# Kernel optimization log

Measured on AMD Instinct MI355X. Metric: run time of the kernel, lower is better.

The kernel has to match this reference:

```python
import jax, jax.numpy as jnp
import numpy as np

N_HEAD = 16

def _alibi_slopes(num_heads):
    # m_i = (256 ** (1/num_heads)) ** -(i+1)
    x = (2.0 ** 8) ** (1.0 / num_heads)
    return jnp.asarray([1.0 / x ** (i + 1) for i in range(num_heads)], dtype=jnp.float32)

def setup_inputs() -> dict:
    key = jax.random.key(0)
    k1, k2 = jax.random.split(key)
    B, S, D = 2, 2048, 1024
    x = jax.random.normal(k1, (B, S, D), dtype=jnp.float32)
    W_kqv = jax.random.normal(k2, (D, 3 * D), dtype=jnp.float32) * 0.02
    return {"x": x, "W_kqv": W_kqv}

def reference(x, W_kqv):
    B, S, D = x.shape
    H = N_HEAD
    hd = D // H
    scale = jnp.sqrt(jnp.asarray(D, dtype=x.dtype))  # NOTE: sqrt(n_embd), per source
    kqv = x @ W_kqv                                   # [B,S,3D]
    k, q, v = jnp.split(kqv, 3, axis=-1)              # chunk order: key, query, value
    q = q.reshape(B, S, H, hd).transpose(0, 2, 1, 3)  # [B,H,S,hd]
    k = k.reshape(B, S, H, hd).transpose(0, 2, 1, 3)
    v = v.reshape(B, S, H, hd).transpose(0, 2, 1, 3)
    # ALiBi bias: m[h] * (j - i)
    pos = jnp.arange(S)
    rel = (pos[None, :] - pos[:, None]).astype(x.dtype)      # [S,S]
    m = _alibi_slopes(H).astype(x.dtype)                     # [H]
    bias = m[:, None, None] * rel                            # [H,S,S]
    score = jnp.einsum('bhqd,bhkd->bhqk', q, k) / scale + bias[None]
    causal = pos[None, :] <= pos[:, None]                    # [S,S] lower-tri
    score = jnp.where(causal[None, None], score, -jnp.inf)
    attn = jax.nn.softmax(score, axis=-1)                    # [B,H,S,S]
    out = jnp.einsum('bhqk,bhkd->bhqd', attn, v)
    out = out.transpose(0, 2, 1, 3).reshape(B, S, D)
    return (out, attn)
```

## Files before the change

### kernel.cpp

```cpp
#include <hip/hip_runtime.h>
#include <hip/hip_bf16.h>

typedef __attribute__((ext_vector_type(8))) short short8;
typedef __attribute__((ext_vector_type(4))) float f32x4;

static __device__ __forceinline__ unsigned short f2bf(float f) {
    unsigned int x = __float_as_uint(f);
    x += 0x7fffu + ((x >> 16) & 1u);
    return (unsigned short)(x >> 16);
}

static __device__ __forceinline__ void gld_lds16(const unsigned short* g, unsigned short* l) {
    __builtin_amdgcn_global_load_lds((const __attribute__((address_space(1))) void*)g,
                                     (__attribute__((address_space(3))) void*)l, 16, 0, 0);
}

__global__ __launch_bounds__(256) void cvt_x_kernel(const float* __restrict__ in,
                                                    unsigned short* __restrict__ outb,
                                                    int n4) {
    int i = blockIdx.x * 256 + threadIdx.x;
    if (i < n4) {
        f32x4 v = *(const f32x4*)(in + (size_t)i * 4);
        ushort4 o;
        o.x = f2bf(v[0]); o.y = f2bf(v[1]); o.z = f2bf(v[2]); o.w = f2bf(v[3]);
        *(ushort4*)(outb + (size_t)i * 4) = o;
    }
}

__global__ __launch_bounds__(256) void cvt_wt_kernel(const float* __restrict__ W,
                                                     unsigned short* __restrict__ WT) {
    __shared__ float t[64][65];
    const int n0 = blockIdx.x * 64;
    const int k0 = blockIdx.y * 64;
    const int tid = threadIdx.x;
#pragma unroll
    for (int i = 0; i < 16; ++i) {
        int lin = tid + i * 256;
        int rr = lin >> 6, cc = lin & 63;
        t[rr][cc] = W[(size_t)(k0 + rr) * 3072 + n0 + cc];
    }
    __syncthreads();
#pragma unroll
    for (int i = 0; i < 16; ++i) {
        int lin = tid + i * 256;
        int nn = lin >> 6, kk = lin & 63;
        WT[(size_t)(n0 + nn) * 1024 + k0 + kk] = f2bf(t[kk][nn]);
    }
}

__global__ __launch_bounds__(256) void gemm_kqv_kernel(
    const unsigned short* __restrict__ A,
    const unsigned short* __restrict__ BT,
    unsigned short* __restrict__ qb,
    unsigned short* __restrict__ kb,
    unsigned short* __restrict__ vtb) {
    __shared__ __attribute__((aligned(16))) unsigned short smem[2 * 128 * 72];
    unsigned short (*As)[64] = (unsigned short(*)[64])smem;
    unsigned short (*Bs)[64] = (unsigned short(*)[64])(smem + 128 * 64);
    const int tid = threadIdx.x;
    const int w = tid >> 6, lane = tid & 63;
    const int quad = lane >> 4, cl = lane & 15;

    const int wg = (int)blockIdx.x + 24 * (int)blockIdx.y;
    const int wgs = (wg & 7) * 96 + (wg >> 3);
    const int m0 = (wgs / 24) * 128, n0 = (wgs % 24) * 128;
    const int wm = (w >> 1) * 64, wn = (w & 1) * 64;

    const int srow = lane >> 3;
    const int schk = (lane & 7) ^ srow;
    const unsigned short* Ap = A + (size_t)(m0 + w * 32 + srow) * 1024 + schk * 8;
    const unsigned short* Bp = BT + (size_t)(n0 + w * 32 + srow) * 1024 + schk * 8;

    f32x4 acc[4][4] = {};

    for (int kk = 0; kk < 1024; kk += 64) {
#pragma unroll
        for (int i = 0; i < 4; ++i) {
            gld_lds16(Ap + kk + (size_t)i * 8 * 1024, &As[w * 32 + i * 8][0]);
            gld_lds16(Bp + kk + (size_t)i * 8 * 1024, &Bs[w * 32 + i * 8][0]);
        }
        __syncthreads();
#pragma unroll
        for (int kc = 0; kc < 2; ++kc) {
            short8 af[4], bfr[4];
#pragma unroll
            for (int i = 0; i < 4; ++i) {
                const int col = ((kc * 4 + quad) ^ (cl & 7)) * 8;
                af[i] = *(const short8*)&As[wm + i * 16 + cl][col];
                bfr[i] = *(const short8*)&Bs[wn + i * 16 + cl][col];
            }
#pragma unroll
            for (int im = 0; im < 4; ++im)
#pragma unroll
                for (int in = 0; in < 4; ++in)
                    acc[im][in] = __builtin_amdgcn_mfma_f32_16x16x32_bf16(
                        af[im], bfr[in], acc[im][in], 0, 0, 0);
        }
        __syncthreads();
    }
    unsigned short (*Cs)[130] = (unsigned short(*)[130])smem;

    const int chunk = n0 >> 10;
    const int d0 = n0 & 1023;
    const int b = m0 >> 11;
    const int s_base = m0 & 2047;

    if (chunk == 2) {
#pragma unroll
        for (int im = 0; im < 4; ++im)
#pragma unroll
            for (int in = 0; in < 4; ++in)
#pragma unroll
                for (int rg = 0; rg < 4; ++rg)
                    Cs[wn + in * 16 + cl][wm + im * 16 + quad * 4 + rg] =
                        f2bf(acc[im][in][rg]);
        __syncthreads();
#pragma unroll
        for (int it = 0; it < 8; ++it) {
            int l = it * 2048 + tid * 8;
            int c = l >> 7;
            int r = l & 127;
            int d = d0 + c, hh = d >> 6, dd = d & 63;
            size_t dst = ((size_t)(b * 16 + hh) * 64 + dd) * 2048 + s_base + r;
            *(uint4*)(vtb + dst) = *(const uint4*)&Cs[c][r];
        }
    } else {
#pragma unroll
        for (int im = 0; im < 4; ++im)
#pragma unroll
            for (int in = 0; in < 4; ++in)
#pragma unroll
                for (int rg = 0; rg < 4; ++rg)
                    Cs[wm + im * 16 + quad * 4 + rg][wn + in * 16 + cl] =
                        f2bf(acc[im][in][rg]);
        __syncthreads();
        unsigned short* outp = (chunk == 0) ? kb : qb;
#pragma unroll
        for (int it = 0; it < 8; ++it) {
            int l = it * 2048 + tid * 8;
            int r = l >> 7;
            int c = l & 127;
            int d = d0 + c, hh = d >> 6, dd = d & 63;
            size_t dst = ((size_t)(b * 16 + hh) * 2048 + s_base + r) * 64 + dd;
            *(uint4*)(outp + dst) = *(const uint4*)&Cs[r][c];
        }
    }
}

__global__ __launch_bounds__(128, 3) void attn_kernel(
    const unsigned short* __restrict__ qb,
    const unsigned short* __restrict__ kb,
    const unsigned short* __restrict__ vtb,
    float* __restrict__ out_,
    float* __restrict__ attn) {
    const int h = blockIdx.y;
    const int b = blockIdx.z;
    const int bh = b * 16 + h;
    const int t32 = (37 * (int)blockIdx.x + 11 * bh) & 63;
    const int tid = threadIdx.x;
    const int w = tid >> 6;
    const int lane = tid & 63;
    const int quad = lane >> 4;
    const int cl = lane & 15;
    const int q0 = t32 * 32;
    const int row0 = q0 + w * 16;
    const int jtmax = t32 >> 1;

    const unsigned short* Qh = qb + (size_t)bh * 2048 * 64;
    const unsigned short* Kh = kb + (size_t)bh * 2048 * 64;
    const unsigned short* Vh = vtb + (size_t)bh * 64 * 2048;
    float* attnh = attn + (size_t)bh * 2048 * 2048;

    short8 aq0 = *(const short8*)(Qh + (size_t)(row0 + cl) * 64 + quad * 8);
    short8 aq1 = *(const short8*)(Qh + (size_t)(row0 + cl) * 64 + 32 + quad * 8);

    const float LOG2E = 1.44269504088896f;
    const float C1 = LOG2E / 32.0f;
    const float M2 = exp2f(-0.5f * (float)(h + 1)) * LOG2E;

    auto loadK = [&](int jt, short8 (&kf)[8]) {
#pragma unroll
        for (int nt = 0; nt < 4; ++nt) {
            const unsigned short* Kp = Kh + (size_t)(jt * 64 + nt * 16 + cl) * 64 + quad * 8;
            kf[nt * 2] = *(const short8*)(Kp);
            kf[nt * 2 + 1] = *(const short8*)(Kp + 32);
        }
    };

    float rsum[4] = {0.f, 0.f, 0.f, 0.f};
    auto tile1 = [&](int jt, const short8 (&kf)[8]) {
        const int j0 = jt * 64;
#pragma unroll
        for (int nt = 0; nt < 4; ++nt) {
            f32x4 s = {0.f, 0.f, 0.f, 0.f};
            s = __builtin_amdgcn_mfma_f32_16x16x32_bf16(aq0, kf[nt * 2], s, 0, 0, 0);
            s = __builtin_amdgcn_mfma_f32_16x16x32_bf16(aq1, kf[nt * 2 + 1], s, 0, 0, 0);
            const int jc = j0 + nt * 16 + cl;
#pragma unroll
            for (int rg = 0; rg < 4; ++rg) {
                int irow = row0 + quad * 4 + rg;
                if (jc <= irow)
                    rsum[rg] += exp2f(s[rg] * C1 + M2 * (float)(jc - irow));
            }
        }
    };

    {
        short8 kf0[8], kf1[8];
        loadK(0, kf0);
        int jt = 0;
        for (;;) {
            if (jt < jtmax) loadK(jt + 1, kf1);
            tile1(jt, kf0);
            if (++jt > jtmax) break;
            if (jt < jtmax) loadK(jt + 1, kf0);
            tile1(jt, kf1);
            if (++jt > jtmax) break;
        }
    }
#pragma unroll
    for (int rg = 0; rg < 4; ++rg) {
        float v = rsum[rg];
        v += __shfl_xor(v, 1);
        v += __shfl_xor(v, 2);
        v += __shfl_xor(v, 4);
        v += __shfl_xor(v, 8);
        rsum[rg] = 1.0f / v;
    }

    __shared__ unsigned short Ps[2][16][72];
    f32x4 oacc[4] = {};
    short8 kf[8], vf[8];
    loadK(0, kf);
    for (int jt = 0; jt <= jtmax; ++jt) {
        const int j0 = jt * 64;
#pragma unroll
        for (int on = 0; on < 4; ++on) {
            const unsigned short* Vp = Vh + (size_t)(on * 16 + cl) * 2048 + j0 + quad * 8;
            vf[on * 2] = *(const short8*)(Vp);
            vf[on * 2 + 1] = *(const short8*)(Vp + 32);
        }
        f32x4 sv[4];
#pragma unroll
        for (int nt = 0; nt < 4; ++nt) {
            f32x4 s = {0.f, 0.f, 0.f, 0.f};
            s = __builtin_amdgcn_mfma_f32_16x16x32_bf16(aq0, kf[nt * 2], s, 0, 0, 0);
            sv[nt] = __builtin_amdgcn_mfma_f32_16x16x32_bf16(aq1, kf[nt * 2 + 1], s, 0, 0, 0);
        }
        if (jt < jtmax) loadK(jt + 1, kf);

#pragma unroll
        for (int nt = 0; nt < 4; ++nt) {
            const int jc = j0 + nt * 16 + cl;
#pragma unroll
            for (int rg = 0; rg < 4; ++rg) {
                const int irow = row0 + quad * 4 + rg;
                float p = (jc <= irow)
                              ? exp2f(sv[nt][rg] * C1 + M2 * (float)(jc - irow)) * rsum[rg]
                              : 0.f;
                Ps[w][quad * 4 + rg][nt * 16 + cl] = f2bf(p);
                __builtin_nontemporal_store(p, attnh + (size_t)irow * 2048 + jc);
            }
        }

        short8 pa0 = *(const short8*)&Ps[w][cl][quad * 8];
        short8 pa1 = *(const short8*)&Ps[w][cl][32 + quad * 8];

#pragma unroll
        for (int on = 0; on < 4; ++on) {
            oacc[on] = __builtin_amdgcn_mfma_f32_16x16x32_bf16(pa0, vf[on * 2], oacc[on], 0, 0, 0);
            oacc[on] = __builtin_amdgcn_mfma_f32_16x16x32_bf16(pa1, vf[on * 2 + 1], oacc[on], 0, 0, 0);
        }
    }

#pragma unroll
    for (int on = 0; on < 4; ++on) {
#pragma unroll
        for (int rg = 0; rg < 4; ++rg) {
            int srow = row0 + quad * 4 + rg;
            __builtin_nontemporal_store(
                oacc[on][rg], out_ + ((size_t)b * 2048 + srow) * 1024 + h * 64 + on * 16 + cl);
        }
    }

    const int jz = (jtmax + 1) * 64;
    if (jz < 2048) {
        f32x4 z = {0.f, 0.f, 0.f, 0.f};
        for (int rr = 0; rr < 16; ++rr) {
            float* dst = attnh + (size_t)(row0 + rr) * 2048;
            for (int c = jz + lane * 4; c < 2048; c += 256)
                __builtin_nontemporal_store(z, (f32x4*)(dst + c));
        }
    }
}

extern "C" void kernel_launch(void* const* d_in, const int* in_sizes, int n_in,
                              void* d_out, int out_size, void* d_ws, size_t ws_size,
                              hipStream_t stream) {
    const float* x = (const float*)d_in[0];
    const float* Wk = (const float*)d_in[1];
    float* out = (float*)d_out;
    float* attn = out + (size_t)2 * 2048 * 1024;

    unsigned short* xb = (unsigned short*)d_ws;
    unsigned short* wtb = xb + (size_t)4096 * 1024;
    unsigned short* qb = wtb + (size_t)3072 * 1024;
    unsigned short* kb = qb + (size_t)32 * 2048 * 64;
    unsigned short* vtb = kb + (size_t)32 * 2048 * 64;

    cvt_x_kernel<<<dim3(4096), dim3(256), 0, stream>>>(x, xb, 4096 * 1024 / 4);
    cvt_wt_kernel<<<dim3(48, 16), dim3(256), 0, stream>>>(Wk, wtb);
    gemm_kqv_kernel<<<dim3(24, 32), dim3(256), 0, stream>>>(xb, wtb, qb, kb, vtb);
    attn_kernel<<<dim3(64, 16, 2), dim3(128), 0, stream>>>(qb, kb, vtb, out, attn);
}
```

Measured before the change: 755.7 us.

## Share K/V tiles across four waves via LDS with async global-to-LDS loads

Attention blocks grow from 2 to 4 waves covering 64 query rows. K and V tiles are staged cooperatively into XOR-swizzled shared memory with global_load_lds, replacing per-wave direct register loads, so each K/V tile is fetched from global memory once per block. The aim is to cut redundant global traffic. In exchange it adds __syncthreads barriers and drops the register double-buffering prefetch. exp2f with pre-scaled constants is also replaced by __expf.

```diff
diff --git a/kernel.cpp b/kernel.cpp
--- a/kernel.cpp
+++ b/kernel.cpp
@@ -147,7 +147,7 @@
     }
 }
 
-__global__ __launch_bounds__(128, 3) void attn_kernel(
+__global__ __launch_bounds__(256, 4) void attn_kernel(
     const unsigned short* __restrict__ qb,
     const unsigned short* __restrict__ kb,
     const unsigned short* __restrict__ vtb,
@@ -156,67 +156,59 @@
     const int h = blockIdx.y;
     const int b = blockIdx.z;
     const int bh = b * 16 + h;
-    const int t32 = (37 * (int)blockIdx.x + 11 * bh) & 63;
+    const int t64 = (23 * (int)blockIdx.x + 7 * bh) & 31;
     const int tid = threadIdx.x;
     const int w = tid >> 6;
     const int lane = tid & 63;
     const int quad = lane >> 4;
     const int cl = lane & 15;
-    const int q0 = t32 * 32;
+    const int q0 = t64 * 64;
     const int row0 = q0 + w * 16;
-    const int jtmax = t32 >> 1;
+    const int jtmax = t64;
 
     const unsigned short* Qh = qb + (size_t)bh * 2048 * 64;
     const unsigned short* Kh = kb + (size_t)bh * 2048 * 64;
     const unsigned short* Vh = vtb + (size_t)bh * 64 * 2048;
     float* attnh = attn + (size_t)bh * 2048 * 2048;
 
+    __shared__ __attribute__((aligned(16))) unsigned short Kt[64][64];
+    __shared__ __attribute__((aligned(16))) unsigned short Vt[64][64];
+    __shared__ unsigned short Ps[4][16][72];
+
+    const int srow = lane >> 3;
+    const int schk = (lane & 7) ^ srow;
+
     short8 aq0 = *(const short8*)(Qh + (size_t)(row0 + cl) * 64 + quad * 8);
     short8 aq1 = *(const short8*)(Qh + (size_t)(row0 + cl) * 64 + 32 + quad * 8);
 
-    const float LOG2E = 1.44269504088896f;
-    const float C1 = LOG2E / 32.0f;
-    const float M2 = exp2f(-0.5f * (float)(h + 1)) * LOG2E;
-
-    auto loadK = [&](int jt, short8 (&kf)[8]) {
+    const float mh = exp2f(-0.5f * (float)(h + 1));
+    const float sc1 = 1.0f / 32.0f;
+
+    float rsum[4] = {0.f, 0.f, 0.f, 0.f};
+    for (int jt = 0; jt <= jtmax; ++jt) {
+        const int j0 = jt * 64;
+#pragma unroll
+        for (int i = 0; i < 2; ++i)
+            gld_lds16(Kh + (size_t)(j0 + w * 16 + i * 8 + srow) * 64 + schk * 8,
+                      &Kt[w * 16 + i * 8][0]);
+        __syncthreads();
 #pragma unroll
         for (int nt = 0; nt < 4; ++nt) {
-            const unsigned short* Kp = Kh + (size_t)(jt * 64 + nt * 16 + cl) * 64 + quad * 8;
-            kf[nt * 2] = *(const short8*)(Kp);
-            kf[nt * 2 + 1] = *(const short8*)(Kp + 32);
-        }
-    };
-
-    float rsum[4] = {0.f, 0.f, 0.f, 0.f};
-    auto tile1 = [&](int jt, const short8 (&kf)[8]) {
-        const int j0 = jt * 64;
-#pragma unroll
-        for (int nt = 0; nt < 4; ++nt) {
+            const int r = nt * 16 + cl;
+            short8 k0 = *(const short8*)&Kt[r][((quad) ^ (cl & 7)) * 8];
+            short8 k1 = *(const short8*)&Kt[r][((quad + 4) ^ (cl & 7)) * 8];
             f32x4 s = {0.f, 0.f, 0.f, 0.f};
-            s = __builtin_amdgcn_mfma_f32_16x16x32_bf16(aq0, kf[nt * 2], s, 0, 0, 0);
-            s = __builtin_amdgcn_mfma_f32_16x16x32_bf16(aq1, kf[nt * 2 + 1], s, 0, 0, 0);
+            s = __builtin_amdgcn_mfma_f32_16x16x32_bf16(aq0, k0, s, 0, 0, 0);
+            s = __builtin_amdgcn_mfma_f32_16x16x32_bf16(aq1, k1, s, 0, 0, 0);
             const int jc = j0 + nt * 16 + cl;
 #pragma unroll
             for (int rg = 0; rg < 4; ++rg) {
                 int irow = row0 + quad * 4 + rg;
                 if (jc <= irow)
-                    rsum[rg] += exp2f(s[rg] * C1 + M2 * (float)(jc - irow));
+                    rsum[rg] += __expf(s[rg] * sc1 + mh * (float)(jc - irow));
             }
         }
-    };
-
-    {
-        short8 kf0[8], kf1[8];
-        loadK(0, kf0);
-        int jt = 0;
-        for (;;) {
-            if (jt < jtmax) loadK(jt + 1, kf1);
-            tile1(jt, kf0);
-            if (++jt > jtmax) break;
-            if (jt < jtmax) loadK(jt + 1, kf0);
-            tile1(jt, kf1);
-            if (++jt > jtmax) break;
-        }
+        __syncthreads();
     }
 #pragma unroll
     for (int rg = 0; rg < 4; ++rg) {
@@ -228,27 +220,27 @@
         rsum[rg] = 1.0f / v;
     }
 
-    __shared__ unsigned short Ps[2][16][72];
     f32x4 oacc[4] = {};
-    short8 kf[8], vf[8];
-    loadK(0, kf);
     for (int jt = 0; jt <= jtmax; ++jt) {
         const int j0 = jt * 64;
 #pragma unroll
-        for (int on = 0; on < 4; ++on) {
-            const unsigned short* Vp = Vh + (size_t)(on * 16 + cl) * 2048 + j0 + quad * 8;
-            vf[on * 2] = *(const short8*)(Vp);
-            vf[on * 2 + 1] = *(const short8*)(Vp + 32);
-        }
+        for (int i = 0; i < 2; ++i) {
+            gld_lds16(Kh + (size_t)(j0 + w * 16 + i * 8 + srow) * 64 + schk * 8,
+                      &Kt[w * 16 + i * 8][0]);
+            gld_lds16(Vh + (size_t)(w * 16 + i * 8 + srow) * 2048 + j0 + schk * 8,
+                      &Vt[w * 16 + i * 8][0]);
+        }
+        __syncthreads();
         f32x4 sv[4];
 #pragma unroll
         for (int nt = 0; nt < 4; ++nt) {
+            const int r = nt * 16 + cl;
+            short8 k0 = *(const short8*)&Kt[r][((quad) ^ (cl & 7)) * 8];
+            short8 k1 = *(const short8*)&Kt[r][((quad + 4) ^ (cl & 7)) * 8];
             f32x4 s = {0.f, 0.f, 0.f, 0.f};
-            s = __builtin_amdgcn_mfma_f32_16x16x32_bf16(aq0, kf[nt * 2], s, 0, 0, 0);
-            sv[nt] = __builtin_amdgcn_mfma_f32_16x16x32_bf16(aq1, kf[nt * 2 + 1], s, 0, 0, 0);
-        }
-        if (jt < jtmax) loadK(jt + 1, kf);
-
+            s = __builtin_amdgcn_mfma_f32_16x16x32_bf16(aq0, k0, s, 0, 0, 0);
+            sv[nt] = __builtin_amdgcn_mfma_f32_16x16x32_bf16(aq1, k1, s, 0, 0, 0);
+        }
 #pragma unroll
         for (int nt = 0; nt < 4; ++nt) {
             const int jc = j0 + nt * 16 + cl;
@@ -256,7 +248,7 @@
             for (int rg = 0; rg < 4; ++rg) {
                 const int irow = row0 + quad * 4 + rg;
                 float p = (jc <= irow)
-                              ? exp2f(sv[nt][rg] * C1 + M2 * (float)(jc - irow)) * rsum[rg]
+                              ? __expf(sv[nt][rg] * sc1 + mh * (float)(jc - irow)) * rsum[rg]
                               : 0.f;
                 Ps[w][quad * 4 + rg][nt * 16 + cl] = f2bf(p);
                 __builtin_nontemporal_store(p, attnh + (size_t)irow * 2048 + jc);
@@ -268,18 +260,22 @@
 
 #pragma unroll
         for (int on = 0; on < 4; ++on) {
-            oacc[on] = __builtin_amdgcn_mfma_f32_16x16x32_bf16(pa0, vf[on * 2], oacc[on], 0, 0, 0);
-            oacc[on] = __builtin_amdgcn_mfma_f32_16x16x32_bf16(pa1, vf[on * 2 + 1], oacc[on], 0, 0, 0);
-        }
+            const int r = on * 16 + cl;
+            short8 v0 = *(const short8*)&Vt[r][((quad) ^ (cl & 7)) * 8];
+            short8 v1 = *(const short8*)&Vt[r][((quad + 4) ^ (cl & 7)) * 8];
+            oacc[on] = __builtin_amdgcn_mfma_f32_16x16x32_bf16(pa0, v0, oacc[on], 0, 0, 0);
+            oacc[on] = __builtin_amdgcn_mfma_f32_16x16x32_bf16(pa1, v1, oacc[on], 0, 0, 0);
+        }
+        __syncthreads();
     }
 
 #pragma unroll
     for (int on = 0; on < 4; ++on) {
 #pragma unroll
         for (int rg = 0; rg < 4; ++rg) {
-            int srow = row0 + quad * 4 + rg;
+            int srow2 = row0 + quad * 4 + rg;
             __builtin_nontemporal_store(
-                oacc[on][rg], out_ + ((size_t)b * 2048 + srow) * 1024 + h * 64 + on * 16 + cl);
+                oacc[on][rg], out_ + ((size_t)b * 2048 + srow2) * 1024 + h * 64 + on * 16 + cl);
         }
     }
 
@@ -311,5 +307,5 @@
     cvt_x_kernel<<<dim3(4096), dim3(256), 0, stream>>>(x, xb, 4096 * 1024 / 4);
     cvt_wt_kernel<<<dim3(48, 16), dim3(256), 0, stream>>>(Wk, wtb);
     gemm_kqv_kernel<<<dim3(24, 32), dim3(256), 0, stream>>>(xb, wtb, qb, kb, vtb);
-    attn_kernel<<<dim3(64, 16, 2), dim3(128), 0, stream>>>(qb, kb, vtb, out, attn);
-}
+    attn_kernel<<<dim3(32, 16, 2), dim3(256), 0, stream>>>(qb, kb, vtb, out, attn);
+}
```

After: 703.2 us. 1.07x faster.
